# Optimization experiments

Hardware: AMD Instinct MI355X
Metric: run time of the kernel (lower is better)

## Reference

```python
import jax, jax.numpy as jnp
import numpy as np

N = 100000   # nodes
E = 1600000  # edges (before self-loops)
IN, HID, OUT = 128, 16, 10
NEG_SLOPE = 0.2
LN_EPS = 1e-5


def layer_norm(x, gamma, beta):
    mu = jnp.mean(x, axis=-1, keepdims=True)
    var = jnp.mean((x - mu) ** 2, axis=-1, keepdims=True)
    return (x - mu) * jax.lax.rsqrt(var + LN_EPS) * gamma + beta


def gat_conv(x, edge_index, W, a_src, a_dst, bias, concat):
    # x: [N, Din], W: [Din, H*F], a_src/a_dst: [H, F]
    n = x.shape[0]
    H, F = a_src.shape
    h = (x @ W).reshape(n, H, F)                      # [N, H, F]
    src, dst = edge_index[0], edge_index[1]
    alpha_src = jnp.sum(h * a_src, axis=-1)           # [N, H]
    alpha_dst = jnp.sum(h * a_dst, axis=-1)           # [N, H]
    e = jax.nn.leaky_relu(alpha_src[src] + alpha_dst[dst], NEG_SLOPE)  # [E, H]
    # segment softmax over incoming edges of each dst node (self-loops guarantee non-empty)
    m = jax.ops.segment_max(e, dst, num_segments=n)
    e = jnp.exp(e - m[dst])
    s = jax.ops.segment_sum(e, dst, num_segments=n)
    alpha = e / (s[dst] + 1e-16)                      # [E, H]
    out = jax.ops.segment_sum(h[src] * alpha[:, :, None], dst, num_segments=n)  # [N, H, F]
    out = out.reshape(n, H * F) if concat else out.mean(axis=1)
    return out + bias


def setup_inputs() -> dict:
    key = jax.random.key(0)
    ks = jax.random.split(key, 20)
    d = {}
    d["x"] = jax.random.normal(ks[0], (N, IN), dtype=jnp.float32)
    d["edge_index"] = jax.random.randint(ks[1], (2, E), 0, N, dtype=jnp.int64)
    s = 0.1
    # layer 1: IN -> HID, 8 heads, concat
    d["W1"] = jax.random.normal(ks[2], (IN, 8 * HID), jnp.float32) * s
    d["a_src1"] = jax.random.normal(ks[3], (8, HID), jnp.float32) * s
    d["a_dst1"] = jax.random.normal(ks[4], (8, HID), jnp.float32) * s
    d["b1"] = jnp.zeros((8 * HID,), jnp.float32)
    d["g1"] = jnp.ones((8 * HID,), jnp.float32)
    d["be1"] = jnp.zeros((8 * HID,), jnp.float32)
    # layer 2: 8*HID -> HID, 4 heads, concat
    d["W2"] = jax.random.normal(ks[5], (8 * HID, 4 * HID), jnp.float32) * s
    d["a_src2"] = jax.random.normal(ks[6], (4, HID), jnp.float32) * s
    d["a_dst2"] = jax.random.normal(ks[7], (4, HID), jnp.float32) * s
    d["b2"] = jnp.zeros((4 * HID,), jnp.float32)
    d["g2"] = jnp.ones((4 * HID,), jnp.float32)
    d["be2"] = jnp.zeros((4 * HID,), jnp.float32)
    # layer 3: 4*HID -> OUT, 1 head, no concat
    d["W3"] = jax.random.normal(ks[8], (4 * HID, OUT), jnp.float32) * s
    d["a_src3"] = jax.random.normal(ks[9], (1, OUT), jnp.float32) * s
    d["a_dst3"] = jax.random.normal(ks[10], (1, OUT), jnp.float32) * s
    d["b3"] = jnp.zeros((OUT,), jnp.float32)
    return d


def reference(x, edge_index, W1, a_src1, a_dst1, b1, g1, be1,
              W2, a_src2, a_dst2, b2, g2, be2,
              W3, a_src3, a_dst3, b3):
    n = x.shape[0]
    loops = jnp.arange(n, dtype=edge_index.dtype)
    ei = jnp.concatenate([edge_index, jnp.stack([loops, loops])], axis=1)  # add self-loops
    h = gat_conv(x, ei, W1, a_src1, a_dst1, b1, concat=True)
    h = jax.nn.elu(layer_norm(h, g1, be1))
    h = gat_conv(h, ei, W2, a_src2, a_dst2, b2, concat=True)
    h = jax.nn.elu(layer_norm(h, g2, be2))
    h = gat_conv(h, ei, W3, a_src3, a_dst3, b3, concat=False)
    return jax.nn.log_softmax(h, axis=1)
```

## Files before the change

### kernel.cpp

```cpp
#include <hip/hip_runtime.h>
#include <hip/hip_bf16.h>
#include <math.h>

typedef __hip_bfloat16 bf16;
typedef __bf16 bf16x8 __attribute__((ext_vector_type(8)));
typedef float floatx4 __attribute__((ext_vector_type(4)));

#define CSR_CH  4096
#define CSR_REG 8192

__device__ __forceinline__ unsigned short f2bu(float f) {
    bf16 b = __float2bfloat16(f);
    return __builtin_bit_cast(unsigned short, b);
}
__device__ __forceinline__ float bu2f(unsigned short u) {
    return __uint_as_float(((unsigned)u) << 16);
}

__device__ __forceinline__ void accu4(float* ac, float w, uint4 u) {
    ac[0] += w * __uint_as_float(u.x << 16);
    ac[1] += w * __uint_as_float(u.x & 0xffff0000u);
    ac[2] += w * __uint_as_float(u.y << 16);
    ac[3] += w * __uint_as_float(u.y & 0xffff0000u);
    ac[4] += w * __uint_as_float(u.z << 16);
    ac[5] += w * __uint_as_float(u.z & 0xffff0000u);
    ac[6] += w * __uint_as_float(u.w << 16);
    ac[7] += w * __uint_as_float(u.w & 0xffff0000u);
}
__device__ __forceinline__ void accu2(float* ac, float w, uint2 u) {
    ac[0] += w * __uint_as_float(u.x << 16);
    ac[1] += w * __uint_as_float(u.x & 0xffff0000u);
    ac[2] += w * __uint_as_float(u.y << 16);
    ac[3] += w * __uint_as_float(u.y & 0xffff0000u);
}

__device__ __forceinline__ float lrelu_exp(float lg) {
    lg = lg > 0.f ? lg : 0.2f * lg;
    return __expf(lg);
}

template<typename XT, int H>
__global__ __launch_bounds__(256) void gemm_mfma(
    const XT* __restrict__ X, const float* __restrict__ W,
    const float* __restrict__ a_src, const float* __restrict__ a_dst,
    bf16* __restrict__ Hout, float* __restrict__ asrc, float* __restrict__ adst,
    int N, int NG, const int* __restrict__ ei, int E, int DPB,
    int* __restrict__ histM)
{
    constexpr int M = H * 16;
    constexpr int KP = 136;
    constexpr int NT = M / 16;
    constexpr int HPQ = H / 4;
    __shared__ __align__(16) unsigned short Wt[M * KP];
    __shared__ __align__(16) unsigned short As[64 * KP];
    __shared__ float As_s[M], Ad_s[M];
    int tid = threadIdx.x;

    if (blockIdx.x >= NG) {
        int* cnt = (int*)Wt;
        cnt[tid] = 0;
        __syncthreads();
        int blk = blockIdx.x - NG;
        int e0 = blk * CSR_CH;
        int e1 = min(E, e0 + CSR_CH);
        for (int e = e0 + tid; e < e1; e += 256)
            atomicAdd(&cnt[ei[E + e] / DPB], 1);
        __syncthreads();
        histM[blk * 256 + tid] = cnt[tid];
        return;
    }

    int r0 = blockIdx.x * 64;
    for (int i = tid; i < M; i += 256) { As_s[i] = a_src[i]; Ad_s[i] = a_dst[i]; }
    for (int idx = tid; idx < 128 * M; idx += 256) {
        int k = idx / M, m = idx % M;
        Wt[m * KP + k] = f2bu(W[idx]);
    }
    if constexpr (__is_same(XT, float)) {
        for (int idx = tid; idx < 64 * 32; idx += 256) {
            int row = idx >> 5, c4 = (idx & 31) * 4;
            int grow = r0 + row;
            float4 v = make_float4(0.f, 0.f, 0.f, 0.f);
            if (grow < N)
                v = *reinterpret_cast<const float4*>(X + (size_t)grow * 128 + c4);
            unsigned short* a = &As[row * KP + c4];
            a[0] = f2bu(v.x); a[1] = f2bu(v.y); a[2] = f2bu(v.z); a[3] = f2bu(v.w);
        }
    } else {
        for (int idx = tid; idx < 64 * 16; idx += 256) {
            int row = idx >> 4, c8 = (idx & 15) * 8;
            int grow = r0 + row;
            uint4 v = make_uint4(0u, 0u, 0u, 0u);
            if (grow < N)
                v = *reinterpret_cast<const uint4*>((const unsigned short*)X + (size_t)grow * 128 + c8);
            *reinterpret_cast<uint4*>(&As[row * KP + c8]) = v;
        }
    }
    __syncthreads();

    int w = tid >> 6, l = tid & 63, q = l >> 4, c = l & 15;
    floatx4 acc[NT];
    #pragma unroll
    for (int t = 0; t < NT; ++t) acc[t] = (floatx4){0.f, 0.f, 0.f, 0.f};

    #pragma unroll
    for (int kc = 0; kc < 4; ++kc) {
        bf16x8 a = *reinterpret_cast<const bf16x8*>(&As[(w * 16 + c) * KP + kc * 32 + q * 8]);
        #pragma unroll
        for (int t = 0; t < NT; ++t) {
            bf16x8 b = *reinterpret_cast<const bf16x8*>(&Wt[(t * 16 + c) * KP + kc * 32 + q * 8]);
            acc[t] = __builtin_amdgcn_mfma_f32_16x16x32_bf16(a, b, acc[t], 0, 0, 0);
        }
    }
    __syncthreads();
    #pragma unroll
    for (int t = 0; t < NT; ++t)
        #pragma unroll
        for (int r = 0; r < 4; ++r)
            As[(w * 16 + q * 4 + r) * KP + t * 16 + c] = f2bu(acc[t][r]);
    __syncthreads();
    for (int idx = tid; idx < 64 * (M / 8); idx += 256) {
        int row = idx / (M / 8), g = idx % (M / 8);
        int grow = r0 + row;
        if (grow < N)
            *reinterpret_cast<uint4*>(Hout + (size_t)grow * M + g * 8) =
                *reinterpret_cast<const uint4*>(&As[row * KP + g * 8]);
    }
    {
        int r = tid >> 2, qq = tid & 3;
        int grow = r0 + r;
        if (grow < N) {
            #pragma unroll
            for (int hh = 0; hh < HPQ; ++hh) {
                int hd = qq * HPQ + hh;
                float s1 = 0.f, s2 = 0.f;
                #pragma unroll
                for (int f = 0; f < 16; f += 2) {
                    unsigned u = *reinterpret_cast<const unsigned*>(&As[r * KP + hd * 16 + f]);
                    float v0 = __uint_as_float(u << 16);
                    float v1 = __uint_as_float(u & 0xffff0000u);
                    s1 += v0 * As_s[hd * 16 + f] + v1 * As_s[hd * 16 + f + 1];
                    s2 += v0 * Ad_s[hd * 16 + f] + v1 * Ad_s[hd * 16 + f + 1];
                }
                asrc[(size_t)grow * H + hd] = s1;
                adst[(size_t)grow * H + hd] = s2;
            }
        }
    }
}

__global__ __launch_bounds__(256) void csr_colscan(
    const int* __restrict__ histM, int NBLK,
    int* __restrict__ offT, int* __restrict__ btot)
{
    __shared__ int sm[512];
    int b = blockIdx.x;
    int tid = threadIdx.x;
    int i0 = tid, i1 = tid + 256;
    sm[i0] = (i0 < NBLK) ? histM[i0 * 256 + b] : 0;
    sm[i1] = (i1 < NBLK) ? histM[i1 * 256 + b] : 0;
    __syncthreads();
    #pragma unroll
    for (int o = 1; o < 512; o <<= 1) {
        int t0 = (i0 >= o) ? sm[i0 - o] : 0;
        int t1 = (i1 >= o) ? sm[i1 - o] : 0;
        __syncthreads();
        sm[i0] += t0; sm[i1] += t1;
        __syncthreads();
    }
    if (i0 < NBLK) offT[b * NBLK + i0] = b * CSR_REG + ((i0 == 0) ? 0 : sm[i0 - 1]);
    if (i1 < NBLK) offT[b * NBLK + i1] = b * CSR_REG + sm[i1 - 1];
    if (tid == 0) btot[b] = sm[511];
}

__global__ __launch_bounds__(256) void csr_pair_scatter(
    const int* __restrict__ ei, int E, int DPB,
    const int* __restrict__ offT, int NBLK,
    unsigned* __restrict__ pairs)
{
    __shared__ int cnt[256];
    int tid = threadIdx.x;
    int blk = blockIdx.x;
    cnt[tid] = offT[tid * NBLK + blk];
    __syncthreads();
    int e0 = blk * CSR_CH;
    int e1 = min(E, e0 + CSR_CH);
    for (int e = e0 + tid; e < e1; e += 256) {
        int s = ei[e];
        int d = ei[E + e];
        int b = d / DPB;
        int dloc = d - b * DPB;
        int pos = atomicAdd(&cnt[b], 1);
        pairs[pos] = ((unsigned)dloc << 17) | (unsigned)s;
    }
}

__global__ __launch_bounds__(256) void csr_fine(
    const unsigned* __restrict__ pairs, const int* __restrict__ btot,
    int DPB, int N, int2* __restrict__ ptrSE, int* __restrict__ col)
{
    __shared__ int sm[512];
    __shared__ int off[512];
    int b = blockIdx.x;
    int tid = threadIdx.x;
    int base = b * CSR_REG;
    int tot = btot[b];
    int d0 = b * DPB;
    int i0 = tid, i1 = tid + 256;
    sm[i0] = 0; sm[i1] = 0;
    __syncthreads();
    for (int i = tid; i < tot; i += 256)
        atomicAdd(&sm[pairs[base + i] >> 17], 1);
    __syncthreads();
    #pragma unroll
    for (int o = 1; o < 512; o <<= 1) {
        int t0 = (i0 >= o) ? sm[i0 - o] : 0;
        int t1 = (i1 >= o) ? sm[i1 - o] : 0;
        __syncthreads();
        sm[i0] += t0; sm[i1] += t1;
        __syncthreads();
    }
    int s0e = base + ((i0 == 0) ? 0 : sm[i0 - 1]);
    int s1e = base + sm[i1 - 1];
    off[i0] = s0e;
    off[i1] = s1e;
    if (i0 < DPB && d0 + i0 < N) ptrSE[d0 + i0] = make_int2(s0e, base + sm[i0]);
    if (i1 < DPB && d0 + i1 < N) ptrSE[d0 + i1] = make_int2(s1e, base + sm[i1]);
    __syncthreads();
    for (int i = tid; i < tot; i += 256) {
        unsigned p = pairs[base + i];
        int pos = atomicAdd(&off[p >> 17], 1);
        col[pos] = (int)(p & 0x1FFFFu);
    }
}

__global__ __launch_bounds__(256) void agg_ln_l1(
    const int2* __restrict__ ptrSE, const int* __restrict__ col,
    const float* __restrict__ asrc, const float* __restrict__ adst,
    const bf16* __restrict__ hb, const float* __restrict__ bias,
    const float* __restrict__ g, const float* __restrict__ be,
    bf16* __restrict__ out, int N)
{
    int tid = threadIdx.x;
    int sub = tid >> 4, j = tid & 15;
    int d = blockIdx.x * 16 + sub;
    if (d >= N) return;
    int f0 = j * 8;
    int hd = j >> 1;
    int2 se = ptrSE[d];
    int e = se.x, end = se.y;
    float adst_h = adst[d * 8 + hd];
    const unsigned short* hw = (const unsigned short*)hb;
    const unsigned short* hwl = hw + f0;
    const float* as_h = asrc + hd;

    float ac[8];
    #pragma unroll
    for (int p = 0; p < 8; ++p) ac[p] = 0.f;
    float dn;

    {
        float w = lrelu_exp(as_h[(size_t)d * 8] + adst_h);
        uint4 u = *reinterpret_cast<const uint4*>(hwl + ((size_t)d << 7));
        accu4(ac, w, u);
        dn = w;
    }

    int cB0 = 0, cB1 = 0, cB2 = 0, cB3 = 0;
    float lA0, lA1, lA2, lA3;
    uint4 uA0, uA1, uA2, uA3;
    if (e + 4 <= end) {
        int a0 = col[e], a1 = col[e + 1], a2 = col[e + 2], a3 = col[e + 3];
        if (e + 8 <= end) { cB0 = col[e + 4]; cB1 = col[e + 5]; cB2 = col[e + 6]; cB3 = col[e + 7]; }
        lA0 = as_h[(size_t)a0 * 8]; lA1 = as_h[(size_t)a1 * 8];
        lA2 = as_h[(size_t)a2 * 8]; lA3 = as_h[(size_t)a3 * 8];
        uA0 = *reinterpret_cast<const uint4*>(hwl + ((size_t)a0 << 7));
        uA1 = *reinterpret_cast<const uint4*>(hwl + ((size_t)a1 << 7));
        uA2 = *reinterpret_cast<const uint4*>(hwl + ((size_t)a2 << 7));
        uA3 = *reinterpret_cast<const uint4*>(hwl + ((size_t)a3 << 7));
    }
    while (e + 4 <= end) {
        int en = e + 4;
        bool hN = (en + 4 <= end);
        int cC0 = cB0, cC1 = cB1, cC2 = cB2, cC3 = cB3;
        if (en + 8 <= end) { cC0 = col[en + 4]; cC1 = col[en + 5]; cC2 = col[en + 6]; cC3 = col[en + 7]; }
        float lB0, lB1, lB2, lB3;
        uint4 uB0, uB1, uB2, uB3;
        if (hN) {
            lB0 = as_h[(size_t)cB0 * 8]; lB1 = as_h[(size_t)cB1 * 8];
            lB2 = as_h[(size_t)cB2 * 8]; lB3 = as_h[(size_t)cB3 * 8];
            uB0 = *reinterpret_cast<const uint4*>(hwl + ((size_t)cB0 << 7));
            uB1 = *reinterpret_cast<const uint4*>(hwl + ((size_t)cB1 << 7));
            uB2 = *reinterpret_cast<const uint4*>(hwl + ((size_t)cB2 << 7));
            uB3 = *reinterpret_cast<const uint4*>(hwl + ((size_t)cB3 << 7));
        }
        float w0 = lrelu_exp(lA0 + adst_h);
        float w1 = lrelu_exp(lA1 + adst_h);
        float w2 = lrelu_exp(lA2 + adst_h);
        float w3 = lrelu_exp(lA3 + adst_h);
        accu4(ac, w0, uA0); accu4(ac, w1, uA1);
        accu4(ac, w2, uA2); accu4(ac, w3, uA3);
        dn += w0 + w1 + w2 + w3;
        cB0 = cC0; cB1 = cC1; cB2 = cC2; cB3 = cC3;
        lA0 = lB0; lA1 = lB1; lA2 = lB2; lA3 = lB3;
        uA0 = uB0; uA1 = uB1; uA2 = uB2; uA3 = uB3;
        e = en;
    }
    for (; e < end; ++e) {
        int s = col[e];
        float w = lrelu_exp(as_h[(size_t)s * 8] + adst_h);
        uint4 u = *reinterpret_cast<const uint4*>(hwl + ((size_t)s << 7));
        accu4(ac, w, u);
        dn += w;
    }

    float rden = 1.f / (dn + 1e-16f);
    float o[8];
    float sm1 = 0.f, sm2 = 0.f;
    #pragma unroll
    for (int p = 0; p < 8; ++p) {
        o[p] = ac[p] * rden + bias[f0 + p];
        sm1 += o[p];
        sm2 += o[p] * o[p];
    }
    #pragma unroll
    for (int off = 8; off >= 1; off >>= 1) {
        sm1 += __shfl_xor(sm1, off, 16);
        sm2 += __shfl_xor(sm2, off, 16);
    }
    float mu = sm1 * (1.f / 128.f);
    float var = sm2 * (1.f / 128.f) - mu * mu;
    float inv = rsqrtf(var + 1e-5f);
    unsigned pk[4];
    #pragma unroll
    for (int p = 0; p < 8; p += 2) {
        float y0 = (o[p] - mu) * inv * g[f0 + p] + be[f0 + p];
        float y1 = (o[p + 1] - mu) * inv * g[f0 + p + 1] + be[f0 + p + 1];
        y0 = y0 > 0.f ? y0 : expm1f(y0);
        y1 = y1 > 0.f ? y1 : expm1f(y1);
        pk[p / 2] = (unsigned)f2bu(y0) | ((unsigned)f2bu(y1) << 16);
    }
    unsigned short* op = (unsigned short*)out + (size_t)d * 128 + f0;
    *reinterpret_cast<uint4*>(op) = make_uint4(pk[0], pk[1], pk[2], pk[3]);
}

__global__ __launch_bounds__(256) void agg_ln_l2_g3(
    const int2* __restrict__ ptrSE, const int* __restrict__ col,
    const float* __restrict__ asrc, const float* __restrict__ adst,
    const bf16* __restrict__ hb, const float* __restrict__ bias,
    const float* __restrict__ g, const float* __restrict__ be,
    const float* __restrict__ W3, const float* __restrict__ as3,
    const float* __restrict__ ad3,
    bf16* __restrict__ h3, float* __restrict__ asrc3, float* __restrict__ adst3,
    int N)
{
    __shared__ float Wl[640], s3[10], d3[10];
    int tid = threadIdx.x;
    for (int i = tid; i < 640; i += 256) Wl[i] = W3[i];
    if (tid < 10) { s3[tid] = as3[tid]; d3[tid] = ad3[tid]; }
    __syncthreads();
    int sub = tid >> 3, j = tid & 7;
    int d = blockIdx.x * 32 + sub;
    if (d >= N) return;
    int f0 = j * 8;
    int hd = j >> 1;
    int2 se = ptrSE[d];
    int e = se.x, end = se.y;
    float adst_h = adst[d * 4 + hd];
    const unsigned short* hw = (const unsigned short*)hb;
    const unsigned short* hwl = hw + f0;
    const float* as_h = asrc + hd;

    float ac[8];
    #pragma unroll
    for (int p = 0; p < 8; ++p) ac[p] = 0.f;
    float dn;

    {
        float w = lrelu_exp(as_h[(size_t)d * 4] + adst_h);
        uint4 u = *reinterpret_cast<const uint4*>(hwl + ((size_t)d << 6));
        accu4(ac, w, u);
        dn = w;
    }

    int cB0 = 0, cB1 = 0, cB2 = 0, cB3 = 0;
    float lA0, lA1, lA2, lA3;
    uint4 uA0, uA1, uA2, uA3;
    if (e + 4 <= end) {
        int a0 = col[e], a1 = col[e + 1], a2 = col[e + 2], a3 = col[e + 3];
        if (e + 8 <= end) { cB0 = col[e + 4]; cB1 = col[e + 5]; cB2 = col[e + 6]; cB3 = col[e + 7]; }
        lA0 = as_h[(size_t)a0 * 4]; lA1 = as_h[(size_t)a1 * 4];
        lA2 = as_h[(size_t)a2 * 4]; lA3 = as_h[(size_t)a3 * 4];
        uA0 = *reinterpret_cast<const uint4*>(hwl + ((size_t)a0 << 6));
        uA1 = *reinterpret_cast<const uint4*>(hwl + ((size_t)a1 << 6));
        uA2 = *reinterpret_cast<const uint4*>(hwl + ((size_t)a2 << 6));
        uA3 = *reinterpret_cast<const uint4*>(hwl + ((size_t)a3 << 6));
    }
    while (e + 4 <= end) {
        int en = e + 4;
        bool hN = (en + 4 <= end);
        int cC0 = cB0, cC1 = cB1, cC2 = cB2, cC3 = cB3;
        if (en + 8 <= end) { cC0 = col[en + 4]; cC1 = col[en + 5]; cC2 = col[en + 6]; cC3 = col[en + 7]; }
        float lB0, lB1, lB2, lB3;
        uint4 uB0, uB1, uB2, uB3;
        if (hN) {
            lB0 = as_h[(size_t)cB0 * 4]; lB1 = as_h[(size_t)cB1 * 4];
            lB2 = as_h[(size_t)cB2 * 4]; lB3 = as_h[(size_t)cB3 * 4];
            uB0 = *reinterpret_cast<const uint4*>(hwl + ((size_t)cB0 << 6));
            uB1 = *reinterpret_cast<const uint4*>(hwl + ((size_t)cB1 << 6));
            uB2 = *reinterpret_cast<const uint4*>(hwl + ((size_t)cB2 << 6));
            uB3 = *reinterpret_cast<const uint4*>(hwl + ((size_t)cB3 << 6));
        }
        float w0 = lrelu_exp(lA0 + adst_h);
        float w1 = lrelu_exp(lA1 + adst_h);
        float w2 = lrelu_exp(lA2 + adst_h);
        float w3 = lrelu_exp(lA3 + adst_h);
        accu4(ac, w0, uA0); accu4(ac, w1, uA1);
        accu4(ac, w2, uA2); accu4(ac, w3, uA3);
        dn += w0 + w1 + w2 + w3;
        cB0 = cC0; cB1 = cC1; cB2 = cC2; cB3 = cC3;
        lA0 = lB0; lA1 = lB1; lA2 = lB2; lA3 = lB3;
        uA0 = uB0; uA1 = uB1; uA2 = uB2; uA3 = uB3;
        e = en;
    }
    for (; e < end; ++e) {
        int s = col[e];
        float w = lrelu_exp(as_h[(size_t)s * 4] + adst_h);
        uint4 u = *reinterpret_cast<const uint4*>(hwl + ((size_t)s << 6));
        accu4(ac, w, u);
        dn += w;
    }

    float rden = 1.f / (dn + 1e-16f);
    float o[8];
    float sm1 = 0.f, sm2 = 0.f;
    #pragma unroll
    for (int p = 0; p < 8; ++p) {
        o[p] = ac[p] * rden + bias[f0 + p];
        sm1 += o[p];
        sm2 += o[p] * o[p];
    }
    #pragma unroll
    for (int off = 4; off >= 1; off >>= 1) {
        sm1 += __shfl_xor(sm1, off, 8);
        sm2 += __shfl_xor(sm2, off, 8);
    }
    float mu = sm1 * (1.f / 64.f);
    float var = sm2 * (1.f / 64.f) - mu * mu;
    float inv = rsqrtf(var + 1e-5f);
    float y[8];
    #pragma unroll
    for (int p = 0; p < 8; ++p) {
        float t = (o[p] - mu) * inv * g[f0 + p] + be[f0 + p];
        y[p] = t > 0.f ? t : expm1f(t);
    }
    float pj[10];
    #pragma unroll
    for (int jj = 0; jj < 10; ++jj) {
        float s = 0.f;
        #pragma unroll
        for (int p = 0; p < 8; ++p)
            s += y[p] * Wl[(f0 + p) * 10 + jj];
        pj[jj] = s;
    }
    #pragma unroll
    for (int off = 4; off >= 1; off >>= 1)
        #pragma unroll
        for (int jj = 0; jj < 10; ++jj)
            pj[jj] += __shfl_xor(pj[jj], off, 8);
    if (j == 0) {
        unsigned short* hr = (unsigned short*)h3 + (size_t)d * 16;
        unsigned q0 = (unsigned)f2bu(pj[0]) | ((unsigned)f2bu(pj[1]) << 16);
        unsigned q1 = (unsigned)f2bu(pj[2]) | ((unsigned)f2bu(pj[3]) << 16);
        unsigned q2 = (unsigned)f2bu(pj[4]) | ((unsigned)f2bu(pj[5]) << 16);
        unsigned q3 = (unsigned)f2bu(pj[6]) | ((unsigned)f2bu(pj[7]) << 16);
        unsigned q4 = (unsigned)f2bu(pj[8]) | ((unsigned)f2bu(pj[9]) << 16);
        *reinterpret_cast<uint4*>(hr) = make_uint4(q0, q1, q2, q3);
        *reinterpret_cast<uint4*>(hr + 8) = make_uint4(q4, 0u, 0u, 0u);
        float a1 = 0.f, a2 = 0.f;
        #pragma unroll
        for (int jj = 0; jj < 10; ++jj) {
            a1 += pj[jj] * s3[jj];
            a2 += pj[jj] * d3[jj];
        }
        asrc3[d] = a1;
        adst3[d] = a2;
    }
}

__global__ __launch_bounds__(256) void agg_l3_final(
    const int2* __restrict__ ptrSE, const int* __restrict__ col,
    const float* __restrict__ asrc, const float* __restrict__ adst,
    const bf16* __restrict__ h, const float* __restrict__ b3,
    float* __restrict__ out, int N)
{
    int tid = threadIdx.x;
    int sub = tid >> 2, j = tid & 3;
    int d = blockIdx.x * 64 + sub;
    if (d >= N) return;
    const unsigned short* hu = (const unsigned short*)h;
    const unsigned short* hul = hu + j * 4;
    int2 se = ptrSE[d];
    int e = se.x, end = se.y;
    float adst_d = adst[d];

    float ac[4] = {0.f, 0.f, 0.f, 0.f};
    float dn;
    {
        float w = lrelu_exp(asrc[d] + adst_d);
        uint2 u = *reinterpret_cast<const uint2*>(hul + (size_t)d * 16);
        accu2(ac, w, u);
        dn = w;
    }

    int cB0 = 0, cB1 = 0, cB2 = 0, cB3 = 0;
    float lA0, lA1, lA2, lA3;
    uint2 uA0, uA1, uA2, uA3;
    if (e + 4 <= end) {
        int a0 = col[e], a1 = col[e + 1], a2 = col[e + 2], a3 = col[e + 3];
        if (e + 8 <= end) { cB0 = col[e + 4]; cB1 = col[e + 5]; cB2 = col[e + 6]; cB3 = col[e + 7]; }
        lA0 = asrc[a0]; lA1 = asrc[a1]; lA2 = asrc[a2]; lA3 = asrc[a3];
        uA0 = *reinterpret_cast<const uint2*>(hul + (size_t)a0 * 16);
        uA1 = *reinterpret_cast<const uint2*>(hul + (size_t)a1 * 16);
        uA2 = *reinterpret_cast<const uint2*>(hul + (size_t)a2 * 16);
        uA3 = *reinterpret_cast<const uint2*>(hul + (size_t)a3 * 16);
    }
    while (e + 4 <= end) {
        int en = e + 4;
        bool hN = (en + 4 <= end);
        int cC0 = cB0, cC1 = cB1, cC2 = cB2, cC3 = cB3;
        if (en + 8 <= end) { cC0 = col[en + 4]; cC1 = col[en + 5]; cC2 = col[en + 6]; cC3 = col[en + 7]; }
        float lB0, lB1, lB2, lB3;
        uint2 uB0, uB1, uB2, uB3;
        if (hN) {
            lB0 = asrc[cB0]; lB1 = asrc[cB1]; lB2 = asrc[cB2]; lB3 = asrc[cB3];
            uB0 = *reinterpret_cast<const uint2*>(hul + (size_t)cB0 * 16);
            uB1 = *reinterpret_cast<const uint2*>(hul + (size_t)cB1 * 16);
            uB2 = *reinterpret_cast<const uint2*>(hul + (size_t)cB2 * 16);
            uB3 = *reinterpret_cast<const uint2*>(hul + (size_t)cB3 * 16);
        }
        float w0 = lrelu_exp(lA0 + adst_d);
        float w1 = lrelu_exp(lA1 + adst_d);
        float w2 = lrelu_exp(lA2 + adst_d);
        float w3 = lrelu_exp(lA3 + adst_d);
        accu2(ac, w0, uA0);
        accu2(ac, w1, uA1);
        accu2(ac, w2, uA2);
        accu2(ac, w3, uA3);
        dn += w0 + w1 + w2 + w3;
        cB0 = cC0; cB1 = cC1; cB2 = cC2; cB3 = cC3;
        lA0 = lB0; lA1 = lB1; lA2 = lB2; lA3 = lB3;
        uA0 = uB0; uA1 = uB1; uA2 = uB2; uA3 = uB3;
        e = en;
    }
    for (; e < end; ++e) {
        int s = col[e];
        float w = lrelu_exp(asrc[s] + adst_d);
        uint2 u = *reinterpret_cast<const uint2*>(hul + (size_t)s * 16);
        accu2(ac, w, u);
        dn += w;
    }

    float rden = 1.f / (dn + 1e-16f);
    int base = j * 4;
    float lv[4];
    #pragma unroll
    for (int p = 0; p < 4; ++p) {
        int idx = base + p;
        float bb = b3[idx < 10 ? idx : 9];
        lv[p] = (idx < 10) ? ac[p] * rden + bb : -1e30f;
    }
    float mx = fmaxf(fmaxf(lv[0], lv[1]), fmaxf(lv[2], lv[3]));
    mx = fmaxf(mx, __shfl_xor(mx, 1, 4));
    mx = fmaxf(mx, __shfl_xor(mx, 2, 4));
    float es = 0.f;
    #pragma unroll
    for (int p = 0; p < 4; ++p)
        es += __expf(lv[p] - mx);
    es += __shfl_xor(es, 1, 4);
    es += __shfl_xor(es, 2, 4);
    float ls = mx + logf(es);
    if (base < 10) {
        float* orow = out + (size_t)d * 10 + base;
        *reinterpret_cast<float2*>(orow) = make_float2(lv[0] - ls, lv[1] - ls);
        if (base + 2 < 10)
            *reinterpret_cast<float2*>(orow + 2) = make_float2(lv[2] - ls, lv[3] - ls);
    }
}

static inline int cdiv(long a, long b) { return (int)((a + b - 1) / b); }

extern "C" void kernel_launch(void* const* d_in, const int* in_sizes, int n_in,
                              void* d_out, int out_size, void* d_ws, size_t ws_size,
                              hipStream_t stream)
{
    const float* x   = (const float*)d_in[0];
    const int*   ei  = (const int*)d_in[1];
    const float* W1  = (const float*)d_in[2];
    const float* as1 = (const float*)d_in[3];
    const float* ad1 = (const float*)d_in[4];
    const float* b1  = (const float*)d_in[5];
    const float* g1  = (const float*)d_in[6];
    const float* be1 = (const float*)d_in[7];
    const float* W2  = (const float*)d_in[8];
    const float* as2 = (const float*)d_in[9];
    const float* ad2 = (const float*)d_in[10];
    const float* b2  = (const float*)d_in[11];
    const float* g2  = (const float*)d_in[12];
    const float* be2 = (const float*)d_in[13];
    const float* W3  = (const float*)d_in[14];
    const float* as3 = (const float*)d_in[15];
    const float* ad3 = (const float*)d_in[16];
    const float* b3  = (const float*)d_in[17];

    const int N = in_sizes[0] / 128;
    const int E = in_sizes[1] / 2;

    const int DPB  = cdiv(N, 256);
    const int NBLK = cdiv(E, CSR_CH);

    bf16*     hb    = (bf16*)d_ws;
    bf16*     aggb  = hb + (size_t)N * 128;
    float*    asrc  = (float*)(aggb + (size_t)N * 128);
    float*    adst  = asrc + (size_t)N * 8;
    float*    asrc3 = adst + (size_t)N * 8;
    float*    adst3 = asrc3 + N;
    unsigned* pairs = (unsigned*)(adst3 + N);
    int*      col   = (int*)(pairs + 256 * CSR_REG);
    int2*     ptrSE = (int2*)(col + 256 * CSR_REG);
    int*      histM = (int*)(ptrSE + N);
    int*      offT  = histM + (size_t)NBLK * 256;
    int*      btot  = offT + (size_t)NBLK * 256;
    bf16*     h3b   = aggb;

    const int NG1 = cdiv(N, 64);

    gemm_mfma<float, 8><<<NG1 + NBLK, 256, 0, stream>>>(
        x, W1, as1, ad1, hb, asrc, adst, N, NG1, ei, E, DPB, histM);
    csr_colscan<<<256, 256, 0, stream>>>(histM, NBLK, offT, btot);
    csr_pair_scatter<<<NBLK, 256, 0, stream>>>(ei, E, DPB, offT, NBLK, pairs);
    csr_fine<<<256, 256, 0, stream>>>(pairs, btot, DPB, N, ptrSE, col);

    agg_ln_l1<<<cdiv(N, 16), 256, 0, stream>>>(
        ptrSE, col, asrc, adst, hb, b1, g1, be1, aggb, N);

    const int NG2 = cdiv(N, 64);
    gemm_mfma<bf16, 4><<<NG2, 256, 0, stream>>>(
        aggb, W2, as2, ad2, hb, asrc, adst, N, NG2, nullptr, 0, 1, nullptr);

    agg_ln_l2_g3<<<cdiv(N, 32), 256, 0, stream>>>(
        ptrSE, col, asrc, adst, hb, b2, g2, be2, W3, as3, ad3,
        h3b, asrc3, adst3, N);

    agg_l3_final<<<cdiv(N, 64), 256, 0, stream>>>(
        ptrSE, col, asrc3, adst3, h3b, b3, (float*)d_out, N);
}
```

Before: 355.3 us.

## Use 1024 CSR buckets with LDS-staged fine sort and deeper gather prefetch

The CSR build now uses 1024 destination buckets of about 98 nodes instead of 256 buckets of about 391, so four times as many blocks run the coarse scan and the fine sort. The fine sort copies each bucket's pairs into shared memory once and reuses them for both the count and the placement passes, which removes a second global read. The layer-1 and layer-2 aggregation loops now prefetch neighbour features two groups ahead instead of one. The cost is more registers in the aggregation kernels, which may lower occupancy, a larger histogram, and a fixed 2048-entry bucket capacity that could overflow for skewed graphs.

```diff
diff --git a/kernel.cpp b/kernel.cpp
--- a/kernel.cpp
+++ b/kernel.cpp
@@ -7,7 +7,8 @@
 typedef float floatx4 __attribute__((ext_vector_type(4)));
 
 #define CSR_CH  4096
-#define CSR_REG 8192
+#define CSR_REG 2048
+#define NBKT    1024
 
 __device__ __forceinline__ unsigned short f2bu(float f) {
     bf16 b = __float2bfloat16(f);
@@ -58,7 +59,7 @@
 
     if (blockIdx.x >= NG) {
         int* cnt = (int*)Wt;
-        cnt[tid] = 0;
+        for (int i = tid; i < NBKT; i += 256) cnt[i] = 0;
         __syncthreads();
         int blk = blockIdx.x - NG;
         int e0 = blk * CSR_CH;
@@ -66,7 +67,7 @@
         for (int e = e0 + tid; e < e1; e += 256)
             atomicAdd(&cnt[ei[E + e] / DPB], 1);
         __syncthreads();
-        histM[blk * 256 + tid] = cnt[tid];
+        for (int i = tid; i < NBKT; i += 256) histM[blk * NBKT + i] = cnt[i];
         return;
     }
 
@@ -157,8 +158,8 @@
     int b = blockIdx.x;
     int tid = threadIdx.x;
     int i0 = tid, i1 = tid + 256;
-    sm[i0] = (i0 < NBLK) ? histM[i0 * 256 + b] : 0;
-    sm[i1] = (i1 < NBLK) ? histM[i1 * 256 + b] : 0;
+    sm[i0] = (i0 < NBLK) ? histM[i0 * NBKT + b] : 0;
+    sm[i1] = (i1 < NBLK) ? histM[i1 * NBKT + b] : 0;
     __syncthreads();
     #pragma unroll
     for (int o = 1; o < 512; o <<= 1) {
@@ -178,10 +179,10 @@
     const int* __restrict__ offT, int NBLK,
     unsigned* __restrict__ pairs)
 {
-    __shared__ int cnt[256];
+    __shared__ int cnt[NBKT];
     int tid = threadIdx.x;
     int blk = blockIdx.x;
-    cnt[tid] = offT[tid * NBLK + blk];
+    for (int i = tid; i < NBKT; i += 256) cnt[i] = offT[i * NBLK + blk];
     __syncthreads();
     int e0 = blk * CSR_CH;
     int e1 = min(E, e0 + CSR_CH);
@@ -199,36 +200,36 @@
     const unsigned* __restrict__ pairs, const int* __restrict__ btot,
     int DPB, int N, int2* __restrict__ ptrSE, int* __restrict__ col)
 {
-    __shared__ int sm[512];
-    __shared__ int off[512];
+    __shared__ int sm[256];
+    __shared__ int off[256];
+    __shared__ unsigned ps[CSR_REG];
     int b = blockIdx.x;
     int tid = threadIdx.x;
     int base = b * CSR_REG;
     int tot = btot[b];
     int d0 = b * DPB;
-    int i0 = tid, i1 = tid + 256;
-    sm[i0] = 0; sm[i1] = 0;
-    __syncthreads();
-    for (int i = tid; i < tot; i += 256)
-        atomicAdd(&sm[pairs[base + i] >> 17], 1);
-    __syncthreads();
-    #pragma unroll
-    for (int o = 1; o < 512; o <<= 1) {
-        int t0 = (i0 >= o) ? sm[i0 - o] : 0;
-        int t1 = (i1 >= o) ? sm[i1 - o] : 0;
-        __syncthreads();
-        sm[i0] += t0; sm[i1] += t1;
-        __syncthreads();
-    }
-    int s0e = base + ((i0 == 0) ? 0 : sm[i0 - 1]);
-    int s1e = base + sm[i1 - 1];
-    off[i0] = s0e;
-    off[i1] = s1e;
-    if (i0 < DPB && d0 + i0 < N) ptrSE[d0 + i0] = make_int2(s0e, base + sm[i0]);
-    if (i1 < DPB && d0 + i1 < N) ptrSE[d0 + i1] = make_int2(s1e, base + sm[i1]);
+    sm[tid] = 0;
     __syncthreads();
     for (int i = tid; i < tot; i += 256) {
         unsigned p = pairs[base + i];
+        ps[i] = p;
+        atomicAdd(&sm[p >> 17], 1);
+    }
+    __syncthreads();
+    #pragma unroll
+    for (int o = 1; o < 256; o <<= 1) {
+        int t = (tid >= o) ? sm[tid - o] : 0;
+        __syncthreads();
+        sm[tid] += t;
+        __syncthreads();
+    }
+    int s_e = base + ((tid == 0) ? 0 : sm[tid - 1]);
+    int e_e = base + sm[tid];
+    off[tid] = s_e;
+    if (tid < DPB && d0 + tid < N) ptrSE[d0 + tid] = make_int2(s_e, e_e);
+    __syncthreads();
+    for (int i = tid; i < tot; i += 256) {
+        unsigned p = ps[i];
         int pos = atomicAdd(&off[p >> 17], 1);
         col[pos] = (int)(p & 0x1FFFFu);
     }
@@ -266,33 +267,46 @@
         dn = w;
     }
 
-    int cB0 = 0, cB1 = 0, cB2 = 0, cB3 = 0;
-    float lA0, lA1, lA2, lA3;
-    uint4 uA0, uA1, uA2, uA3;
+    int cC0 = 0, cC1 = 0, cC2 = 0, cC3 = 0;
+    int cD0 = 0, cD1 = 0, cD2 = 0, cD3 = 0;
+    float lA0 = 0.f, lA1 = 0.f, lA2 = 0.f, lA3 = 0.f;
+    float lB0 = 0.f, lB1 = 0.f, lB2 = 0.f, lB3 = 0.f;
+    float lC0 = 0.f, lC1 = 0.f, lC2 = 0.f, lC3 = 0.f;
+    uint4 uA0 = {}, uA1 = {}, uA2 = {}, uA3 = {};
+    uint4 uB0 = {}, uB1 = {}, uB2 = {}, uB3 = {};
+    uint4 uC0 = {}, uC1 = {}, uC2 = {}, uC3 = {};
     if (e + 4 <= end) {
         int a0 = col[e], a1 = col[e + 1], a2 = col[e + 2], a3 = col[e + 3];
-        if (e + 8 <= end) { cB0 = col[e + 4]; cB1 = col[e + 5]; cB2 = col[e + 6]; cB3 = col[e + 7]; }
+        int b0 = 0, b1 = 0, b2 = 0, b3 = 0;
+        if (e + 8 <= end) { b0 = col[e + 4]; b1 = col[e + 5]; b2 = col[e + 6]; b3 = col[e + 7]; }
+        if (e + 12 <= end) { cC0 = col[e + 8]; cC1 = col[e + 9]; cC2 = col[e + 10]; cC3 = col[e + 11]; }
+        if (e + 16 <= end) { cD0 = col[e + 12]; cD1 = col[e + 13]; cD2 = col[e + 14]; cD3 = col[e + 15]; }
         lA0 = as_h[(size_t)a0 * 8]; lA1 = as_h[(size_t)a1 * 8];
         lA2 = as_h[(size_t)a2 * 8]; lA3 = as_h[(size_t)a3 * 8];
         uA0 = *reinterpret_cast<const uint4*>(hwl + ((size_t)a0 << 7));
         uA1 = *reinterpret_cast<const uint4*>(hwl + ((size_t)a1 << 7));
         uA2 = *reinterpret_cast<const uint4*>(hwl + ((size_t)a2 << 7));
         uA3 = *reinterpret_cast<const uint4*>(hwl + ((size_t)a3 << 7));
+        if (e + 8 <= end) {
+            lB0 = as_h[(size_t)b0 * 8]; lB1 = as_h[(size_t)b1 * 8];
+            lB2 = as_h[(size_t)b2 * 8]; lB3 = as_h[(size_t)b3 * 8];
+            uB0 = *reinterpret_cast<const uint4*>(hwl + ((size_t)b0 << 7));
+            uB1 = *reinterpret_cast<const uint4*>(hwl + ((size_t)b1 << 7));
+            uB2 = *reinterpret_cast<const uint4*>(hwl + ((size_t)b2 << 7));
+            uB3 = *reinterpret_cast<const uint4*>(hwl + ((size_t)b3 << 7));
+        }
     }
     while (e + 4 <= end) {
         int en = e + 4;
-        bool hN = (en + 4 <= end);
-        int cC0 = cB0, cC1 = cB1, cC2 = cB2, cC3 = cB3;
-        if (en + 8 <= end) { cC0 = col[en + 4]; cC1 = col[en + 5]; cC2 = col[en + 6]; cC3 = col[en + 7]; }
-        float lB0, lB1, lB2, lB3;
-        uint4 uB0, uB1, uB2, uB3;
-        if (hN) {
-            lB0 = as_h[(size_t)cB0 * 8]; lB1 = as_h[(size_t)cB1 * 8];
-            lB2 = as_h[(size_t)cB2 * 8]; lB3 = as_h[(size_t)cB3 * 8];
-            uB0 = *reinterpret_cast<const uint4*>(hwl + ((size_t)cB0 << 7));
-            uB1 = *reinterpret_cast<const uint4*>(hwl + ((size_t)cB1 << 7));
-            uB2 = *reinterpret_cast<const uint4*>(hwl + ((size_t)cB2 << 7));
-            uB3 = *reinterpret_cast<const uint4*>(hwl + ((size_t)cB3 << 7));
+        int nE0 = cD0, nE1 = cD1, nE2 = cD2, nE3 = cD3;
+        if (e + 20 <= end) { nE0 = col[e + 16]; nE1 = col[e + 17]; nE2 = col[e + 18]; nE3 = col[e + 19]; }
+        if (e + 12 <= end) {
+            lC0 = as_h[(size_t)cC0 * 8]; lC1 = as_h[(size_t)cC1 * 8];
+            lC2 = as_h[(size_t)cC2 * 8]; lC3 = as_h[(size_t)cC3 * 8];
+            uC0 = *reinterpret_cast<const uint4*>(hwl + ((size_t)cC0 << 7));
+            uC1 = *reinterpret_cast<const uint4*>(hwl + ((size_t)cC1 << 7));
+            uC2 = *reinterpret_cast<const uint4*>(hwl + ((size_t)cC2 << 7));
+            uC3 = *reinterpret_cast<const uint4*>(hwl + ((size_t)cC3 << 7));
         }
         float w0 = lrelu_exp(lA0 + adst_h);
         float w1 = lrelu_exp(lA1 + adst_h);
@@ -301,9 +315,12 @@
         accu4(ac, w0, uA0); accu4(ac, w1, uA1);
         accu4(ac, w2, uA2); accu4(ac, w3, uA3);
         dn += w0 + w1 + w2 + w3;
-        cB0 = cC0; cB1 = cC1; cB2 = cC2; cB3 = cC3;
         lA0 = lB0; lA1 = lB1; lA2 = lB2; lA3 = lB3;
         uA0 = uB0; uA1 = uB1; uA2 = uB2; uA3 = uB3;
+        lB0 = lC0; lB1 = lC1; lB2 = lC2; lB3 = lC3;
+        uB0 = uC0; uB1 = uC1; uB2 = uC2; uB3 = uC3;
+        cC0 = cD0; cC1 = cD1; cC2 = cD2; cC3 = cD3;
+        cD0 = nE0; cD1 = nE1; cD2 = nE2; cD3 = nE3;
         e = en;
     }
     for (; e < end; ++e) {
@@ -383,33 +400,46 @@
         dn = w;
     }
 
-    int cB0 = 0, cB1 = 0, cB2 = 0, cB3 = 0;
-    float lA0, lA1, lA2, lA3;
-    uint4 uA0, uA1, uA2, uA3;
+    int cC0 = 0, cC1 = 0, cC2 = 0, cC3 = 0;
+    int cD0 = 0, cD1 = 0, cD2 = 0, cD3 = 0;
+    float lA0 = 0.f, lA1 = 0.f, lA2 = 0.f, lA3 = 0.f;
+    float lB0 = 0.f, lB1 = 0.f, lB2 = 0.f, lB3 = 0.f;
+    float lC0 = 0.f, lC1 = 0.f, lC2 = 0.f, lC3 = 0.f;
+    uint4 uA0 = {}, uA1 = {}, uA2 = {}, uA3 = {};
+    uint4 uB0 = {}, uB1 = {}, uB2 = {}, uB3 = {};
+    uint4 uC0 = {}, uC1 = {}, uC2 = {}, uC3 = {};
     if (e + 4 <= end) {
         int a0 = col[e], a1 = col[e + 1], a2 = col[e + 2], a3 = col[e + 3];
-        if (e + 8 <= end) { cB0 = col[e + 4]; cB1 = col[e + 5]; cB2 = col[e + 6]; cB3 = col[e + 7]; }
+        int b0 = 0, b1 = 0, b2 = 0, b3 = 0;
+        if (e + 8 <= end) { b0 = col[e + 4]; b1 = col[e + 5]; b2 = col[e + 6]; b3 = col[e + 7]; }
+        if (e + 12 <= end) { cC0 = col[e + 8]; cC1 = col[e + 9]; cC2 = col[e + 10]; cC3 = col[e + 11]; }
+        if (e + 16 <= end) { cD0 = col[e + 12]; cD1 = col[e + 13]; cD2 = col[e + 14]; cD3 = col[e + 15]; }
         lA0 = as_h[(size_t)a0 * 4]; lA1 = as_h[(size_t)a1 * 4];
         lA2 = as_h[(size_t)a2 * 4]; lA3 = as_h[(size_t)a3 * 4];
         uA0 = *reinterpret_cast<const uint4*>(hwl + ((size_t)a0 << 6));
         uA1 = *reinterpret_cast<const uint4*>(hwl + ((size_t)a1 << 6));
         uA2 = *reinterpret_cast<const uint4*>(hwl + ((size_t)a2 << 6));
         uA3 = *reinterpret_cast<const uint4*>(hwl + ((size_t)a3 << 6));
+        if (e + 8 <= end) {
+            lB0 = as_h[(size_t)b0 * 4]; lB1 = as_h[(size_t)b1 * 4];
+            lB2 = as_h[(size_t)b2 * 4]; lB3 = as_h[(size_t)b3 * 4];
+            uB0 = *reinterpret_cast<const uint4*>(hwl + ((size_t)b0 << 6));
+            uB1 = *reinterpret_cast<const uint4*>(hwl + ((size_t)b1 << 6));
+            uB2 = *reinterpret_cast<const uint4*>(hwl + ((size_t)b2 << 6));
+            uB3 = *reinterpret_cast<const uint4*>(hwl + ((size_t)b3 << 6));
+        }
     }
     while (e + 4 <= end) {
         int en = e + 4;
-        bool hN = (en + 4 <= end);
-        int cC0 = cB0, cC1 = cB1, cC2 = cB2, cC3 = cB3;
-        if (en + 8 <= end) { cC0 = col[en + 4]; cC1 = col[en + 5]; cC2 = col[en + 6]; cC3 = col[en + 7]; }
-        float lB0, lB1, lB2, lB3;
-        uint4 uB0, uB1, uB2, uB3;
-        if (hN) {
-            lB0 = as_h[(size_t)cB0 * 4]; lB1 = as_h[(size_t)cB1 * 4];
-            lB2 = as_h[(size_t)cB2 * 4]; lB3 = as_h[(size_t)cB3 * 4];
-            uB0 = *reinterpret_cast<const uint4*>(hwl + ((size_t)cB0 << 6));
-            uB1 = *reinterpret_cast<const uint4*>(hwl + ((size_t)cB1 << 6));
-            uB2 = *reinterpret_cast<const uint4*>(hwl + ((size_t)cB2 << 6));
-            uB3 = *reinterpret_cast<const uint4*>(hwl + ((size_t)cB3 << 6));
+        int nE0 = cD0, nE1 = cD1, nE2 = cD2, nE3 = cD3;
+        if (e + 20 <= end) { nE0 = col[e + 16]; nE1 = col[e + 17]; nE2 = col[e + 18]; nE3 = col[e + 19]; }
+        if (e + 12 <= end) {
+            lC0 = as_h[(size_t)cC0 * 4]; lC1 = as_h[(size_t)cC1 * 4];
+            lC2 = as_h[(size_t)cC2 * 4]; lC3 = as_h[(size_t)cC3 * 4];
+            uC0 = *reinterpret_cast<const uint4*>(hwl + ((size_t)cC0 << 6));
+            uC1 = *reinterpret_cast<const uint4*>(hwl + ((size_t)cC1 << 6));
+            uC2 = *reinterpret_cast<const uint4*>(hwl + ((size_t)cC2 << 6));
+            uC3 = *reinterpret_cast<const uint4*>(hwl + ((size_t)cC3 << 6));
         }
         float w0 = lrelu_exp(lA0 + adst_h);
         float w1 = lrelu_exp(lA1 + adst_h);
@@ -418,9 +448,12 @@
         accu4(ac, w0, uA0); accu4(ac, w1, uA1);
         accu4(ac, w2, uA2); accu4(ac, w3, uA3);
         dn += w0 + w1 + w2 + w3;
-        cB0 = cC0; cB1 = cC1; cB2 = cC2; cB3 = cC3;
         lA0 = lB0; lA1 = lB1; lA2 = lB2; lA3 = lB3;
         uA0 = uB0; uA1 = uB1; uA2 = uB2; uA3 = uB3;
+        lB0 = lC0; lB1 = lC1; lB2 = lC2; lB3 = lC3;
+        uB0 = uC0; uB1 = uC1; uB2 = uC2; uB3 = uC3;
+        cC0 = cD0; cC1 = cD1; cC2 = cD2; cC3 = cD3;
+        cD0 = nE0; cD1 = nE1; cD2 = nE2; cD3 = nE3;
         e = en;
     }
     for (; e < end; ++e) {
@@ -616,7 +649,7 @@
     const int N = in_sizes[0] / 128;
     const int E = in_sizes[1] / 2;
 
-    const int DPB  = cdiv(N, 256);
+    const int DPB  = cdiv(N, NBKT);
     const int NBLK = cdiv(E, CSR_CH);
 
     bf16*     hb    = (bf16*)d_ws;
@@ -626,20 +659,20 @@
     float*    asrc3 = adst + (size_t)N * 8;
     float*    adst3 = asrc3 + N;
     unsigned* pairs = (unsigned*)(adst3 + N);
-    int*      col   = (int*)(pairs + 256 * CSR_REG);
-    int2*     ptrSE = (int2*)(col + 256 * CSR_REG);
+    int*      col   = (int*)(pairs + (size_t)NBKT * CSR_REG);
+    int2*     ptrSE = (int2*)(col + (size_t)NBKT * CSR_REG);
     int*      histM = (int*)(ptrSE + N);
-    int*      offT  = histM + (size_t)NBLK * 256;
-    int*      btot  = offT + (size_t)NBLK * 256;
+    int*      offT  = histM + (size_t)NBLK * NBKT;
+    int*      btot  = offT + (size_t)NBKT * NBLK;
     bf16*     h3b   = aggb;
 
     const int NG1 = cdiv(N, 64);
 
     gemm_mfma<float, 8><<<NG1 + NBLK, 256, 0, stream>>>(
         x, W1, as1, ad1, hb, asrc, adst, N, NG1, ei, E, DPB, histM);
-    csr_colscan<<<256, 256, 0, stream>>>(histM, NBLK, offT, btot);
+    csr_colscan<<<NBKT, 256, 0, stream>>>(histM, NBLK, offT, btot);
     csr_pair_scatter<<<NBLK, 256, 0, stream>>>(ei, E, DPB, offT, NBLK, pairs);
-    csr_fine<<<256, 256, 0, stream>>>(pairs, btot, DPB, N, ptrSE, col);
+    csr_fine<<<NBKT, 256, 0, stream>>>(pairs, btot, DPB, N, ptrSE, col);
 
     agg_ln_l1<<<cdiv(N, 16), 256, 0, stream>>>(
         ptrSE, col, asrc, adst, hb, b1, g1, be1, aggb, N);
```

After: 376.2 us. 1.06x slower.

## Replace two-level bucketed CSR build with global atomic histogram, scan, scatter

Applied to the files above, without the earlier changes.

The CSR construction changes from a two-level bucket scheme (per-chunk LDS histograms, a column scan, pair scatter, then a per-bucket fine sort in LDS) to a direct per-node global atomic histogram. That histogram is followed by a three-kernel prefix scan and a scatter using global atomicAdd on per-node offsets. It drops the intermediate pairs buffer and the fine pass, but replaces LDS atomics with about 1.6M global atomics, used twice. Column order within each row becomes nondeterministic. The kernel count stays similar, with a memset added.

```diff
diff --git a/kernel.cpp b/kernel.cpp
--- a/kernel.cpp
+++ b/kernel.cpp
@@ -7,7 +7,6 @@
 typedef float floatx4 __attribute__((ext_vector_type(4)));
 
 #define CSR_CH  4096
-#define CSR_REG 8192
 
 __device__ __forceinline__ unsigned short f2bu(float f) {
     bf16 b = __float2bfloat16(f);
@@ -44,8 +43,8 @@
     const XT* __restrict__ X, const float* __restrict__ W,
     const float* __restrict__ a_src, const float* __restrict__ a_dst,
     bf16* __restrict__ Hout, float* __restrict__ asrc, float* __restrict__ adst,
-    int N, int NG, const int* __restrict__ ei, int E, int DPB,
-    int* __restrict__ histM)
+    int N, int NG, const int* __restrict__ ei, int E,
+    int* __restrict__ cnt)
 {
     constexpr int M = H * 16;
     constexpr int KP = 136;
@@ -57,16 +56,11 @@
     int tid = threadIdx.x;
 
     if (blockIdx.x >= NG) {
-        int* cnt = (int*)Wt;
-        cnt[tid] = 0;
-        __syncthreads();
         int blk = blockIdx.x - NG;
         int e0 = blk * CSR_CH;
         int e1 = min(E, e0 + CSR_CH);
         for (int e = e0 + tid; e < e1; e += 256)
-            atomicAdd(&cnt[ei[E + e] / DPB], 1);
-        __syncthreads();
-        histM[blk * 256 + tid] = cnt[tid];
+            atomicAdd(&cnt[ei[E + e]], 1);
         return;
     }
 
@@ -149,88 +143,72 @@
     }
 }
 
-__global__ __launch_bounds__(256) void csr_colscan(
-    const int* __restrict__ histM, int NBLK,
-    int* __restrict__ offT, int* __restrict__ btot)
+__global__ __launch_bounds__(256) void csr_scanA(
+    const int* __restrict__ cnt, int N, int* __restrict__ bsum)
+{
+    __shared__ int sm[256];
+    int b = blockIdx.x, t = threadIdx.x, i = b * 256 + t;
+    sm[t] = (i < N) ? cnt[i] : 0;
+    __syncthreads();
+    #pragma unroll
+    for (int o = 128; o > 0; o >>= 1) {
+        if (t < o) sm[t] += sm[t + o];
+        __syncthreads();
+    }
+    if (t == 0) bsum[b] = sm[0];
+}
+
+__global__ __launch_bounds__(512) void csr_scanB(
+    const int* __restrict__ bsum, int NCH, int* __restrict__ boff)
 {
     __shared__ int sm[512];
-    int b = blockIdx.x;
-    int tid = threadIdx.x;
-    int i0 = tid, i1 = tid + 256;
-    sm[i0] = (i0 < NBLK) ? histM[i0 * 256 + b] : 0;
-    sm[i1] = (i1 < NBLK) ? histM[i1 * 256 + b] : 0;
+    int t = threadIdx.x;
+    sm[t] = (t < NCH) ? bsum[t] : 0;
     __syncthreads();
     #pragma unroll
     for (int o = 1; o < 512; o <<= 1) {
-        int t0 = (i0 >= o) ? sm[i0 - o] : 0;
-        int t1 = (i1 >= o) ? sm[i1 - o] : 0;
+        int x = (t >= o) ? sm[t - o] : 0;
         __syncthreads();
-        sm[i0] += t0; sm[i1] += t1;
+        sm[t] += x;
         __syncthreads();
     }
-    if (i0 < NBLK) offT[b * NBLK + i0] = b * CSR_REG + ((i0 == 0) ? 0 : sm[i0 - 1]);
-    if (i1 < NBLK) offT[b * NBLK + i1] = b * CSR_REG + sm[i1 - 1];
-    if (tid == 0) btot[b] = sm[511];
-}
-
-__global__ __launch_bounds__(256) void csr_pair_scatter(
-    const int* __restrict__ ei, int E, int DPB,
-    const int* __restrict__ offT, int NBLK,
-    unsigned* __restrict__ pairs)
-{
-    __shared__ int cnt[256];
-    int tid = threadIdx.x;
-    int blk = blockIdx.x;
-    cnt[tid] = offT[tid * NBLK + blk];
+    if (t < NCH) boff[t] = (t == 0) ? 0 : sm[t - 1];
+}
+
+__global__ __launch_bounds__(256) void csr_scanC(
+    const int* __restrict__ cnt, const int* __restrict__ boff, int N,
+    int* __restrict__ off, int2* __restrict__ ptrSE)
+{
+    __shared__ int sm[256];
+    int b = blockIdx.x, t = threadIdx.x, i = b * 256 + t;
+    int v = (i < N) ? cnt[i] : 0;
+    sm[t] = v;
     __syncthreads();
-    int e0 = blk * CSR_CH;
-    int e1 = min(E, e0 + CSR_CH);
-    for (int e = e0 + tid; e < e1; e += 256) {
+    #pragma unroll
+    for (int o = 1; o < 256; o <<= 1) {
+        int x = (t >= o) ? sm[t - o] : 0;
+        __syncthreads();
+        sm[t] += x;
+        __syncthreads();
+    }
+    if (i < N) {
+        int start = boff[b] + sm[t] - v;
+        off[i] = start;
+        ptrSE[i] = make_int2(start, start + v);
+    }
+}
+
+__global__ __launch_bounds__(256) void csr_scatter(
+    const int* __restrict__ ei, int E,
+    int* __restrict__ off, int* __restrict__ col)
+{
+    int idx = blockIdx.x * 256 + threadIdx.x;
+    int stride = gridDim.x * 256;
+    for (int e = idx; e < E; e += stride) {
         int s = ei[e];
         int d = ei[E + e];
-        int b = d / DPB;
-        int dloc = d - b * DPB;
-        int pos = atomicAdd(&cnt[b], 1);
-        pairs[pos] = ((unsigned)dloc << 17) | (unsigned)s;
-    }
-}
-
-__global__ __launch_bounds__(256) void csr_fine(
-    const unsigned* __restrict__ pairs, const int* __restrict__ btot,
-    int DPB, int N, int2* __restrict__ ptrSE, int* __restrict__ col)
-{
-    __shared__ int sm[512];
-    __shared__ int off[512];
-    int b = blockIdx.x;
-    int tid = threadIdx.x;
-    int base = b * CSR_REG;
-    int tot = btot[b];
-    int d0 = b * DPB;
-    int i0 = tid, i1 = tid + 256;
-    sm[i0] = 0; sm[i1] = 0;
-    __syncthreads();
-    for (int i = tid; i < tot; i += 256)
-        atomicAdd(&sm[pairs[base + i] >> 17], 1);
-    __syncthreads();
-    #pragma unroll
-    for (int o = 1; o < 512; o <<= 1) {
-        int t0 = (i0 >= o) ? sm[i0 - o] : 0;
-        int t1 = (i1 >= o) ? sm[i1 - o] : 0;
-        __syncthreads();
-        sm[i0] += t0; sm[i1] += t1;
-        __syncthreads();
-    }
-    int s0e = base + ((i0 == 0) ? 0 : sm[i0 - 1]);
-    int s1e = base + sm[i1 - 1];
-    off[i0] = s0e;
-    off[i1] = s1e;
-    if (i0 < DPB && d0 + i0 < N) ptrSE[d0 + i0] = make_int2(s0e, base + sm[i0]);
-    if (i1 < DPB && d0 + i1 < N) ptrSE[d0 + i1] = make_int2(s1e, base + sm[i1]);
-    __syncthreads();
-    for (int i = tid; i < tot; i += 256) {
-        unsigned p = pairs[base + i];
-        int pos = atomicAdd(&off[p >> 17], 1);
-        col[pos] = (int)(p & 0x1FFFFu);
+        int pos = atomicAdd(&off[d], 1);
+        col[pos] = s;
     }
 }
 
@@ -616,8 +594,8 @@
     const int N = in_sizes[0] / 128;
     const int E = in_sizes[1] / 2;
 
-    const int DPB  = cdiv(N, 256);
     const int NBLK = cdiv(E, CSR_CH);
+    const int NCH  = cdiv(N, 256);
 
     bf16*     hb    = (bf16*)d_ws;
     bf16*     aggb  = hb + (size_t)N * 128;
@@ -625,28 +603,30 @@
     float*    adst  = asrc + (size_t)N * 8;
     float*    asrc3 = adst + (size_t)N * 8;
     float*    adst3 = asrc3 + N;
-    unsigned* pairs = (unsigned*)(adst3 + N);
-    int*      col   = (int*)(pairs + 256 * CSR_REG);
-    int2*     ptrSE = (int2*)(col + 256 * CSR_REG);
-    int*      histM = (int*)(ptrSE + N);
-    int*      offT  = histM + (size_t)NBLK * 256;
-    int*      btot  = offT + (size_t)NBLK * 256;
+    int*      col   = (int*)(adst3 + N);
+    int2*     ptrSE = (int2*)(col + E);
+    int*      cnt   = (int*)(ptrSE + N);
+    int*      off   = cnt + N;
+    int*      bsum  = off + N;
+    int*      boff  = bsum + NCH;
     bf16*     h3b   = aggb;
 
     const int NG1 = cdiv(N, 64);
 
+    hipMemsetAsync(cnt, 0, (size_t)N * sizeof(int), stream);
     gemm_mfma<float, 8><<<NG1 + NBLK, 256, 0, stream>>>(
-        x, W1, as1, ad1, hb, asrc, adst, N, NG1, ei, E, DPB, histM);
-    csr_colscan<<<256, 256, 0, stream>>>(histM, NBLK, offT, btot);
-    csr_pair_scatter<<<NBLK, 256, 0, stream>>>(ei, E, DPB, offT, NBLK, pairs);
-    csr_fine<<<256, 256, 0, stream>>>(pairs, btot, DPB, N, ptrSE, col);
+        x, W1, as1, ad1, hb, asrc, adst, N, NG1, ei, E, cnt);
+    csr_scanA<<<NCH, 256, 0, stream>>>(cnt, N, bsum);
+    csr_scanB<<<1, 512, 0, stream>>>(bsum, NCH, boff);
+    csr_scanC<<<NCH, 256, 0, stream>>>(cnt, boff, N, off, ptrSE);
+    csr_scatter<<<1024, 256, 0, stream>>>(ei, E, off, col);
 
     agg_ln_l1<<<cdiv(N, 16), 256, 0, stream>>>(
         ptrSE, col, asrc, adst, hb, b1, g1, be1, aggb, N);
 
     const int NG2 = cdiv(N, 64);
     gemm_mfma<bf16, 4><<<NG2, 256, 0, stream>>>(
-        aggb, W2, as2, ad2, hb, asrc, adst, N, NG2, nullptr, 0, 1, nullptr);
+        aggb, W2, as2, ad2, hb, asrc, adst, N, NG2, nullptr, 0, nullptr);
 
     agg_ln_l2_g3<<<cdiv(N, 32), 256, 0, stream>>>(
         ptrSE, col, asrc, adst, hb, b2, g2, be2, W3, as3, ad3,
```

New measurement: 509.8 us. 1.43x slower.
